# Kernel tuning notes

Hardware: AMD Instinct MI355X
Metric: run time of the kernel (lower is better)

The kernel has to match this reference:

```python
import jax, jax.numpy as jnp
import numpy as np

B, N, D = 256, 131072, 256
TEMP = 0.05
EPS_SM = 1e-6
EPS_LOG = 1e-6
NUM_CLUSTERS = 1000


def _l2norm(x):
    return x / jnp.linalg.norm(x, axis=-1, keepdims=True)


def setup_inputs() -> dict:
    key = jax.random.key(0)
    k1, k2, k3, k4, k5 = jax.random.split(key, 5)
    # re-ID features are L2-normalized in practice; keeps exp(logits/temp) finite
    inputs = _l2norm(jax.random.normal(k1, (B, D), jnp.float32))
    indexes = jax.random.randint(k2, (B,), 0, N)
    labels = jax.random.randint(k3, (N,), 0, NUM_CLUSTERS)  # pseudo cluster ids buffer
    cluster_features = _l2norm(jax.random.normal(k4, (N, D), jnp.float32))
    instance_features = _l2norm(jax.random.normal(k5, (N, D), jnp.float32))
    return {
        "inputs": inputs,
        "cluster_features": cluster_features,
        "instance_features": instance_features,
        "indexes": indexes,
        "labels": labels,
    }


def reference(inputs, cluster_features, instance_features, indexes, labels):
    # targets = labels[indexes]
    targets = labels[indexes]
    # bank similarity GEMM, temperature scaling
    logits = jnp.matmul(inputs, cluster_features.T) / TEMP  # [B, N]
    # module's custom softmax: exp / (sum + eps)  (intentionally no max-subtract)
    exps = jnp.exp(logits)
    masked_sim = exps / (jnp.sum(exps, axis=1, keepdims=True) + EPS_SM)
    logp = jnp.log(masked_sim + EPS_LOG)
    # F.nll_loss: mean of -logp at target column
    loss = -jnp.mean(jnp.take_along_axis(logp, targets[:, None], axis=1))
    return loss
```

## Files before the change

kernel.cpp:

```cpp
#include <hip/hip_runtime.h>
#include <hip/hip_bf16.h>
#include <cstdint>

#define B_ 256
#define N_ 131072
#define D_ 256
#define INV_TEMP 20.0f
#define EPS_SM 1e-6f
#define EPS_LOG 1e-6f

#define TPB 512
#define BN 128
#define BK 64
#define TILES 4
#define NBLK (N_ / (TILES * BN))
#define LDB 72
#define BUFE (BN * LDB)

typedef __bf16 bf16_t;
typedef bf16_t bf16x8 __attribute__((ext_vector_type(8)));
typedef float f32x4 __attribute__((ext_vector_type(4)));

__device__ inline ushort f2bf(float f) {
  uint32_t u = __builtin_bit_cast(uint32_t, f);
  u += 0x7FFFu + ((u >> 16) & 1u);
  return (ushort)(u >> 16);
}

__device__ inline void lds_barrier() {
  asm volatile("s_waitcnt lgkmcnt(0)\n\ts_barrier" ::: "memory");
}

__global__ __launch_bounds__(TPB, 2)
void gemm_rowsum(const float* __restrict__ inp, const float* __restrict__ cf,
                 float* __restrict__ rowsum) {
  __shared__ ushort smem[2 * BUFE];
  const int tid  = threadIdx.x;
  const int wave = tid >> 6;
  const int lane = tid & 63;
  const int m15  = lane & 15;
  const int q    = lane >> 4;

  bf16x8 areg[8][2];
#pragma unroll
  for (int kc = 0; kc < 4; ++kc) {
    const int row = tid >> 1, half = tid & 1;
    const float* src = inp + row * D_ + kc * BK + half * 32;
#pragma unroll
    for (int i = 0; i < 8; ++i) {
      const float4 v = *(const float4*)(src + i * 4);
      ushort4 w = {f2bf(v.x), f2bf(v.y), f2bf(v.z), f2bf(v.w)};
      *(ushort4*)(&smem[row * LDB + half * 32 + i * 4]) = w;
    }
    __syncthreads();
#pragma unroll
    for (int mb = 0; mb < 2; ++mb)
#pragma unroll
      for (int ks = 0; ks < 2; ++ks)
        areg[kc * 2 + ks][mb] = __builtin_bit_cast(
            bf16x8, *(const uint4*)(&smem[(wave * 32 + mb * 16 + m15) * LDB + ks * 32 + q * 8]));
    __syncthreads();
  }

  const size_t nbase = (size_t)blockIdx.x * (TILES * BN);
  const int brow = tid >> 2, bcg = tid & 3;

  f32x4 acc[2][8];
  float rs[2][4];
#pragma unroll
  for (int mb = 0; mb < 2; ++mb) {
#pragma unroll
    for (int nb = 0; nb < 8; ++nb) acc[mb][nb] = (f32x4){0.f, 0.f, 0.f, 0.f};
#pragma unroll
    for (int r = 0; r < 4; ++r) rs[mb][r] = 0.f;
  }

  float4 ldbuf[2][4];
#define LDADDR(c) (cf + (nbase + (size_t)((c) >> 2) * BN + brow) * D_ + ((c) & 3) * BK + bcg * 16)

#pragma unroll
  for (int i = 0; i < 4; ++i) ldbuf[0][i] = *(const float4*)(LDADDR(0) + i * 4);
#pragma unroll
  for (int i = 0; i < 4; ++i) ldbuf[1][i] = *(const float4*)(LDADDR(1) + i * 4);
  {
    ushort* dst = &smem[0 * BUFE + brow * LDB + bcg * 16];
#pragma unroll
    for (int i = 0; i < 4; ++i) {
      const float4 v = ldbuf[0][i];
      ushort4 w = {f2bf(v.x), f2bf(v.y), f2bf(v.z), f2bf(v.w)};
      *(ushort4*)(dst + i * 4) = w;
    }
  }

#pragma unroll
  for (int c = 0; c < TILES * 4; ++c) {
    lds_barrier();
    if (c + 2 < TILES * 4) {
#pragma unroll
      for (int i = 0; i < 4; ++i) ldbuf[c & 1][i] = *(const float4*)(LDADDR(c + 2) + i * 4);
    }
    const ushort* bs = &smem[(c & 1) * BUFE];
#pragma unroll
    for (int ks = 0; ks < 2; ++ks) {
      bf16x8 bfr[8];
#pragma unroll
      for (int nb = 0; nb < 8; ++nb)
        bfr[nb] = __builtin_bit_cast(
            bf16x8, *(const uint4*)(&bs[(nb * 16 + m15) * LDB + ks * 32 + q * 8]));
#pragma unroll
      for (int mb = 0; mb < 2; ++mb)
#pragma unroll
        for (int nb = 0; nb < 8; ++nb)
          acc[mb][nb] = __builtin_amdgcn_mfma_f32_16x16x32_bf16(
              areg[(c & 3) * 2 + ks][mb], bfr[nb], acc[mb][nb], 0, 0, 0);
    }
    if ((c & 3) == 3) {
#pragma unroll
      for (int mb = 0; mb < 2; ++mb)
#pragma unroll
        for (int nb = 0; nb < 8; ++nb)
#pragma unroll
          for (int r = 0; r < 4; ++r)
            rs[mb][r] += __expf(acc[mb][nb][r] * INV_TEMP);
      if (c + 1 < TILES * 4) {
#pragma unroll
        for (int mb = 0; mb < 2; ++mb)
#pragma unroll
          for (int nb = 0; nb < 8; ++nb) acc[mb][nb] = (f32x4){0.f, 0.f, 0.f, 0.f};
      }
    }
    if (c + 1 < TILES * 4) {
      ushort* dst = &smem[((c + 1) & 1) * BUFE + brow * LDB + bcg * 16];
#pragma unroll
      for (int i = 0; i < 4; ++i) {
        const float4 v = ldbuf[(c + 1) & 1][i];
        ushort4 w = {f2bf(v.x), f2bf(v.y), f2bf(v.z), f2bf(v.w)};
        *(ushort4*)(dst + i * 4) = w;
      }
    }
  }

#pragma unroll
  for (int off = 8; off >= 1; off >>= 1)
#pragma unroll
    for (int mb = 0; mb < 2; ++mb)
#pragma unroll
      for (int r = 0; r < 4; ++r)
        rs[mb][r] += __shfl_xor(rs[mb][r], off, 64);

  if (m15 == 0) {
    float* slot = rowsum + (size_t)blockIdx.x * B_;
#pragma unroll
    for (int mb = 0; mb < 2; ++mb)
#pragma unroll
      for (int r = 0; r < 4; ++r)
        slot[wave * 32 + mb * 16 + q * 4 + r] = rs[mb][r];
  }
#undef LDADDR
}

__global__ __launch_bounds__(1024)
void finalize_loss(const float* __restrict__ inp, const float* __restrict__ cf,
                   const int* __restrict__ idx, const int* __restrict__ lab,
                   const float* __restrict__ rowsum, float* __restrict__ out) {
  __shared__ float red[1024];
  __shared__ float lg[256];
  const int tid = threadIdx.x;
  const int r = tid & 255, p = tid >> 8;

  const int t = lab[idx[r]];
  const float4* a = (const float4*)(inp + r * D_ + p * 64);
  const float4* c = (const float4*)(cf + (size_t)t * D_ + p * 64);
  float dot = 0.f;
#pragma unroll
  for (int i = 0; i < 16; ++i) {
    const float4 x = a[i], y = c[i];
    dot += x.x * y.x + x.y * y.y + x.z * y.z + x.w * y.w;
  }
  red[tid] = dot;

  float S = 0.f;
#pragma unroll 8
  for (int j = 0; j < NBLK / 4; ++j) S += rowsum[(size_t)(p * (NBLK / 4) + j) * B_ + r];
  __syncthreads();
  const float d4 = red[r] + red[r + 256] + red[r + 512] + red[r + 768];
  __syncthreads();
  red[tid] = S;
  __syncthreads();
  if (tid < 256) {
    const float Sr = red[r] + red[r + 256] + red[r + 512] + red[r + 768];
    lg[r] = __logf(__expf(d4 * INV_TEMP) / (Sr + EPS_SM) + EPS_LOG);
  }
  __syncthreads();
  for (int off = 128; off >= 1; off >>= 1) {
    if (tid < off) lg[tid] += lg[tid + off];
    __syncthreads();
  }
  if (tid == 0) out[0] = -lg[0] * (1.0f / 256.0f);
}

extern "C" void kernel_launch(void* const* d_in, const int* in_sizes, int n_in,
                              void* d_out, int out_size, void* d_ws, size_t ws_size,
                              hipStream_t stream) {
  const float* inp = (const float*)d_in[0];
  const float* cf  = (const float*)d_in[1];
  const int* idx = (const int*)d_in[3];
  const int* lab = (const int*)d_in[4];
  float* out = (float*)d_out;
  float* rowsum = (float*)d_ws;

  gemm_rowsum<<<dim3(NBLK), dim3(TPB), 0, stream>>>(inp, cf, rowsum);
  finalize_loss<<<dim3(1), dim3(1024), 0, stream>>>(inp, cf, idx, lab, rowsum, out);
}
```

Measured before the change: 290.8 us.

## Fuse finalize into GEMM kernel via last-block atomic counter and slotted atomics

Folds the single-block finalize kernel into the GEMM kernel. Blocks atomically add their row sums into 16 slot buffers, and the last block, detected through an atomic counter, computes the loss. The first two B-tile loads are also issued before the A staging, and the A-staging __syncthreads are swapped for the lighter LDS barrier. This removes a separate launch and the large per-block rowsum array, but adds a memset launch and atomic contention on the slots.

```diff
diff --git a/kernel.cpp b/kernel.cpp
--- a/kernel.cpp
+++ b/kernel.cpp
@@ -16,6 +16,7 @@
 #define NBLK (N_ / (TILES * BN))
 #define LDB 72
 #define BUFE (BN * LDB)
+#define NSLOT 16
 
 typedef __bf16 bf16_t;
 typedef bf16_t bf16x8 __attribute__((ext_vector_type(8)));
@@ -32,8 +33,10 @@
 }
 
 __global__ __launch_bounds__(TPB, 2)
-void gemm_rowsum(const float* __restrict__ inp, const float* __restrict__ cf,
-                 float* __restrict__ rowsum) {
+void gemm_fused(const float* __restrict__ inp, const float* __restrict__ cf,
+                const int* __restrict__ idx, const int* __restrict__ lab,
+                float* __restrict__ slots, unsigned int* __restrict__ counter,
+                float* __restrict__ out) {
   __shared__ ushort smem[2 * BUFE];
   const int tid  = threadIdx.x;
   const int wave = tid >> 6;
@@ -41,6 +44,16 @@
   const int m15  = lane & 15;
   const int q    = lane >> 4;
 
+  const size_t nbase = (size_t)blockIdx.x * (TILES * BN);
+  const int brow = tid >> 2, bcg = tid & 3;
+#define LDADDR(c) (cf + (nbase + (size_t)((c) >> 2) * BN + brow) * D_ + ((c) & 3) * BK + bcg * 16)
+
+  float4 ldbuf[2][4];
+#pragma unroll
+  for (int i = 0; i < 4; ++i) ldbuf[0][i] = *(const float4*)(LDADDR(0) + i * 4);
+#pragma unroll
+  for (int i = 0; i < 4; ++i) ldbuf[1][i] = *(const float4*)(LDADDR(1) + i * 4);
+
   bf16x8 areg[8][2];
 #pragma unroll
   for (int kc = 0; kc < 4; ++kc) {
@@ -52,18 +65,15 @@
       ushort4 w = {f2bf(v.x), f2bf(v.y), f2bf(v.z), f2bf(v.w)};
       *(ushort4*)(&smem[row * LDB + half * 32 + i * 4]) = w;
     }
-    __syncthreads();
+    lds_barrier();
 #pragma unroll
     for (int mb = 0; mb < 2; ++mb)
 #pragma unroll
       for (int ks = 0; ks < 2; ++ks)
         areg[kc * 2 + ks][mb] = __builtin_bit_cast(
             bf16x8, *(const uint4*)(&smem[(wave * 32 + mb * 16 + m15) * LDB + ks * 32 + q * 8]));
-    __syncthreads();
-  }
-
-  const size_t nbase = (size_t)blockIdx.x * (TILES * BN);
-  const int brow = tid >> 2, bcg = tid & 3;
+    lds_barrier();
+  }
 
   f32x4 acc[2][8];
   float rs[2][4];
@@ -75,13 +85,6 @@
     for (int r = 0; r < 4; ++r) rs[mb][r] = 0.f;
   }
 
-  float4 ldbuf[2][4];
-#define LDADDR(c) (cf + (nbase + (size_t)((c) >> 2) * BN + brow) * D_ + ((c) & 3) * BK + bcg * 16)
-
-#pragma unroll
-  for (int i = 0; i < 4; ++i) ldbuf[0][i] = *(const float4*)(LDADDR(0) + i * 4);
-#pragma unroll
-  for (int i = 0; i < 4; ++i) ldbuf[1][i] = *(const float4*)(LDADDR(1) + i * 4);
   {
     ushort* dst = &smem[0 * BUFE + brow * LDB + bcg * 16];
 #pragma unroll
@@ -139,6 +142,7 @@
       }
     }
   }
+#undef LDADDR
 
 #pragma unroll
   for (int off = 8; off >= 1; off >>= 1)
@@ -149,54 +153,53 @@
         rs[mb][r] += __shfl_xor(rs[mb][r], off, 64);
 
   if (m15 == 0) {
-    float* slot = rowsum + (size_t)blockIdx.x * B_;
+    float* slot = slots + (blockIdx.x & (NSLOT - 1)) * B_;
 #pragma unroll
     for (int mb = 0; mb < 2; ++mb)
 #pragma unroll
       for (int r = 0; r < 4; ++r)
-        slot[wave * 32 + mb * 16 + q * 4 + r] = rs[mb][r];
-  }
-#undef LDADDR
-}
-
-__global__ __launch_bounds__(1024)
-void finalize_loss(const float* __restrict__ inp, const float* __restrict__ cf,
-                   const int* __restrict__ idx, const int* __restrict__ lab,
-                   const float* __restrict__ rowsum, float* __restrict__ out) {
-  __shared__ float red[1024];
-  __shared__ float lg[256];
-  const int tid = threadIdx.x;
+        atomicAdd(&slot[wave * 32 + mb * 16 + q * 4 + r], rs[mb][r]);
+  }
+
+  __threadfence();
+  __syncthreads();
+  int* flag = (int*)smem;
+  if (tid == 0) {
+    unsigned old = atomicAdd(counter, 1u);
+    flag[4096] = (old == NBLK - 1);
+  }
+  __syncthreads();
+  if (!flag[4096]) return;
+  __threadfence();
+
+  float* sf = (float*)smem;
   const int r = tid & 255, p = tid >> 8;
-
   const int t = lab[idx[r]];
-  const float4* a = (const float4*)(inp + r * D_ + p * 64);
-  const float4* c = (const float4*)(cf + (size_t)t * D_ + p * 64);
+  const float4* a = (const float4*)(inp + r * D_ + p * 128);
+  const float4* cc = (const float4*)(cf + (size_t)t * D_ + p * 128);
   float dot = 0.f;
 #pragma unroll
-  for (int i = 0; i < 16; ++i) {
-    const float4 x = a[i], y = c[i];
+  for (int i = 0; i < 32; ++i) {
+    const float4 x = a[i], y = cc[i];
     dot += x.x * y.x + x.y * y.y + x.z * y.z + x.w * y.w;
   }
-  red[tid] = dot;
-
   float S = 0.f;
-#pragma unroll 8
-  for (int j = 0; j < NBLK / 4; ++j) S += rowsum[(size_t)(p * (NBLK / 4) + j) * B_ + r];
-  __syncthreads();
-  const float d4 = red[r] + red[r + 256] + red[r + 512] + red[r + 768];
-  __syncthreads();
-  red[tid] = S;
+#pragma unroll
+  for (int s = 0; s < NSLOT / 2; ++s) S += slots[(size_t)(p * (NSLOT / 2) + s) * B_ + r];
+  sf[tid] = dot;
+  sf[512 + tid] = S;
   __syncthreads();
   if (tid < 256) {
-    const float Sr = red[r] + red[r + 256] + red[r + 512] + red[r + 768];
-    lg[r] = __logf(__expf(d4 * INV_TEMP) / (Sr + EPS_SM) + EPS_LOG);
+    const float d4 = sf[r] + sf[r + 256];
+    const float Sr = sf[512 + r] + sf[768 + r];
+    sf[1024 + r] = __logf(__expf(d4 * INV_TEMP) / (Sr + EPS_SM) + EPS_LOG);
   }
   __syncthreads();
   for (int off = 128; off >= 1; off >>= 1) {
-    if (tid < off) lg[tid] += lg[tid + off];
+    if (tid < off) sf[1024 + tid] += sf[1024 + tid + off];
     __syncthreads();
   }
-  if (tid == 0) out[0] = -lg[0] * (1.0f / 256.0f);
+  if (tid == 0) out[0] = -sf[1024] * (1.0f / 256.0f);
 }
 
 extern "C" void kernel_launch(void* const* d_in, const int* in_sizes, int n_in,
@@ -207,8 +210,9 @@
   const int* idx = (const int*)d_in[3];
   const int* lab = (const int*)d_in[4];
   float* out = (float*)d_out;
-  float* rowsum = (float*)d_ws;
-
-  gemm_rowsum<<<dim3(NBLK), dim3(TPB), 0, stream>>>(inp, cf, rowsum);
-  finalize_loss<<<dim3(1), dim3(1024), 0, stream>>>(inp, cf, idx, lab, rowsum, out);
-}
+  float* slots = (float*)d_ws;
+  unsigned int* counter = (unsigned int*)(slots + NSLOT * B_);
+
+  hipMemsetAsync(d_ws, 0, NSLOT * B_ * sizeof(float) + sizeof(unsigned int), stream);
+  gemm_fused<<<dim3(NBLK), dim3(TPB), 0, stream>>>(inp, cf, idx, lab, slots, counter, out);
+}
```

Result: slower. 312.4 us (+7.4%).
